# Performance work log

Measured on AMD Instinct MI355X. Metric: run time of the kernel, lower is better.

Reference implementation:

```python
import jax, jax.numpy as jnp
import numpy as np

BN, N, FIN, FO, H = 4, 2048, 128, 64, 4
D = FO * H  # 256


def setup_inputs() -> dict:
    key = jax.random.key(0)
    ks = jax.random.split(key, 13)
    rnd = lambda k, s, sc=1.0: jax.random.normal(k, s, dtype=jnp.float32) * sc
    return {
        "x": rnd(ks[0], (BN, N, FIN)),
        "adj": rnd(ks[1], (BN, N, N)),
        "W_proj": rnd(ks[2], (D, FIN), 0.08),        # xavier-ish scale
        "score_src": rnd(ks[3], (H, FO), 0.1),        # (head_num, out_features)
        "score_tgt": rnd(ks[4], (H, FO), 0.1),
        "bias_out": jnp.zeros((D,), jnp.float32),
        "w_r": rnd(ks[5], (D, D), 0.06),
        "u_r": rnd(ks[6], (D, D), 0.06),
        "w_z": rnd(ks[7], (D, D), 0.06),
        "b_wz": jnp.full((D,), -2.0, jnp.float32),    # GRUGate init_bias
        "u_z": rnd(ks[8], (D, D), 0.06),
        "w_g": rnd(ks[9], (D, D), 0.06),
        "u_g": rnd(ks[10], (D, D), 0.06),
    }


def reference(x, adj, W_proj, score_src, score_tgt, bias_out,
              w_r, u_r, w_z, b_wz, u_z, w_g, u_g):
    bn, n = x.shape[:2]
    h, fo = score_src.shape
    # eval mode: dropout is identity
    proj_flat = x @ W_proj.T                                   # (bn, n, fo*h)
    # reshape splits last dim as (fo, h): head index fastest-varying
    proj = proj_flat.reshape(bn, n, fo, h).transpose(0, 3, 1, 2)  # (bn, h, n, fo)
    residual = proj_flat                                       # (bn, n, fo*h)
    s_src = jnp.einsum('bhnf,hf->bhn', proj, score_src)
    s_tgt = jnp.einsum('bhnf,hf->bhn', proj, score_tgt)
    scores = jax.nn.leaky_relu(s_src[..., :, None] + s_tgt[..., None, :], 0.2)
    scores = scores + adj[:, None]                             # (bn, h, n, n)
    attn = jax.nn.softmax(scores, axis=-1)
    out = jnp.einsum('bhij,bhjf->bhif', attn, proj)            # (bn, h, n, fo)
    out = out.transpose(0, 2, 1, 3).reshape(bn, n, h * fo)
    # GRUGate is computed in the torch source but its result is discarded
    z = jax.nn.sigmoid(out @ w_z.T + b_wz + residual @ u_z.T)
    r = jax.nn.sigmoid(out @ w_r.T + residual @ u_r.T)
    h_hat = jnp.tanh(out @ w_g.T + (r * residual) @ u_g.T)
    _gru = (1.0 - z) * residual + z * h_hat  # unused, matches source bug
    return jax.nn.elu(out + bias_out)
```

## Files before the change

### kernel.cpp

```cpp
#include <hip/hip_runtime.h>
#include <hip/hip_bf16.h>
#include <math.h>

#define BN_   4
#define NN_   2048
#define FIN_  128
#define FO_   64
#define H_    4
#define D_    256

typedef __attribute__((ext_vector_type(8))) short bf16x8;
typedef __attribute__((ext_vector_type(4))) float floatx4;

#define LOG2E 1.4426950408889634f

#if __has_builtin(__builtin_amdgcn_exp2f)
#define EXP2(x) __builtin_amdgcn_exp2f(x)
#else
#define EXP2(x) exp2f(x)
#endif

__device__ __forceinline__ float bf2f(short u) {
    union { unsigned int i; float f; } v;
    v.i = ((unsigned int)(unsigned short)u) << 16;
    return v.f;
}
__device__ __forceinline__ short f2bf(float f) {
    union { float f; unsigned int u; } v; v.f = f;
    unsigned int r = v.u + 0x7fffu + ((v.u >> 16) & 1u);
    return (short)(unsigned short)(r >> 16);
}

#if defined(__BF16_MANT_DIG__)
typedef __bf16 bfr2 __attribute__((ext_vector_type(2)));
__device__ __forceinline__ unsigned int pack_bf16(float a, float b) {
    union { bfr2 h; unsigned int u; } v;
    v.h = (bfr2){(__bf16)a, (__bf16)b};
    return v.u;
}
#else
__device__ __forceinline__ unsigned int pack_bf16(float a, float b) {
    return ((unsigned int)(unsigned short)f2bf(a)) |
           (((unsigned int)(unsigned short)f2bf(b)) << 16);
}
#endif

__device__ __forceinline__ bf16x8 load8f(const float* __restrict__ p) {
    floatx4 a = *(const floatx4*)p;
    floatx4 b = *(const floatx4*)(p + 4);
    union { bf16x8 v; unsigned int u[4]; } r;
    r.u[0] = pack_bf16(a[0], a[1]);
    r.u[1] = pack_bf16(a[2], a[3]);
    r.u[2] = pack_bf16(b[0], b[1]);
    r.u[3] = pack_bf16(b[2], b[3]);
    return r.v;
}

__device__ __forceinline__ float score_exp(float ssv, float stv, float av) {
    float s = ssv + stv;
    s = fmaxf(s, 0.2f * s);
    return EXP2((s + av) * LOG2E);
}

__global__ __launch_bounds__(256) void proj_kernel(
    const float* __restrict__ x,
    const float* __restrict__ wproj,
    const float* __restrict__ ssrc,
    const float* __restrict__ stgt,
    short* __restrict__ pt,
    float* __restrict__ sS,
    float* __restrict__ sT,
    int b0)
{
    __shared__ short ptl[64][264];

    const int tid  = threadIdx.x;
    const int wave = tid >> 6;
    const int lane = tid & 63;
    const int l16  = lane & 15;
    const int quad = lane >> 4;

    const int b_rel = blockIdx.z;
    const int b  = b0 + b_rel;
    const int h  = blockIdx.y;
    const int j0 = blockIdx.x * 256 + wave * 64;

    floatx4 acc[4][4];
#pragma unroll
    for (int mi = 0; mi < 4; ++mi)
#pragma unroll
        for (int nj = 0; nj < 4; ++nj)
            acc[mi][nj] = (floatx4){0.f, 0.f, 0.f, 0.f};

#pragma unroll
    for (int kc = 0; kc < 4; ++kc) {
        const int c = kc * 32 + quad * 8;
        bf16x8 afr[4], bfr[4];
#pragma unroll
        for (int mi = 0; mi < 4; ++mi) {
            int f = mi * 16 + l16;
            int srow = f * H_ + h;
            afr[mi] = load8f(wproj + srow * FIN_ + c);
        }
#pragma unroll
        for (int nj = 0; nj < 4; ++nj) {
            int j = j0 + nj * 16 + l16;
            bfr[nj] = load8f(x + ((size_t)b * NN_ + j) * FIN_ + c);
        }
#pragma unroll
        for (int mi = 0; mi < 4; ++mi)
#pragma unroll
            for (int nj = 0; nj < 4; ++nj)
                acc[mi][nj] = __builtin_amdgcn_mfma_f32_16x16x32_bf16(
                    afr[mi], bfr[nj], acc[mi][nj], 0, 0, 0);
    }

#pragma unroll
    for (int mi = 0; mi < 4; ++mi)
#pragma unroll
        for (int r = 0; r < 4; ++r)
#pragma unroll
            for (int nj = 0; nj < 4; ++nj)
                ptl[mi * 16 + quad * 4 + r][wave * 64 + nj * 16 + l16] =
                    f2bf(acc[mi][nj][r]);

    float wsv[4][4], wtv[4][4];
#pragma unroll
    for (int mi = 0; mi < 4; ++mi)
#pragma unroll
        for (int r = 0; r < 4; ++r) {
            int f = mi * 16 + quad * 4 + r;
            wsv[mi][r] = ssrc[h * FO_ + f];
            wtv[mi][r] = stgt[h * FO_ + f];
        }
    const size_t sbase = ((size_t)b_rel * H_ + h) * NN_;
#pragma unroll
    for (int nj = 0; nj < 4; ++nj) {
        float ps = 0.f, pg = 0.f;
#pragma unroll
        for (int mi = 0; mi < 4; ++mi)
#pragma unroll
            for (int r = 0; r < 4; ++r) {
                ps = fmaf(wsv[mi][r], acc[mi][nj][r], ps);
                pg = fmaf(wtv[mi][r], acc[mi][nj][r], pg);
            }
        ps += __shfl_xor(ps, 16, 64); ps += __shfl_xor(ps, 32, 64);
        pg += __shfl_xor(pg, 16, 64); pg += __shfl_xor(pg, 32, 64);
        if (quad == 0) {
            int j = j0 + nj * 16 + l16;
            sS[sbase + j] = ps;
            sT[sbase + j] = pg;
        }
    }

    __syncthreads();

    const size_t base = ((size_t)b_rel * H_ + h) * (size_t)(64 * 2048)
                      + (size_t)(blockIdx.x * 8) * 2048;
#pragma unroll
    for (int p = 0; p < 8; ++p) {
        const int uid  = p * 256 + tid;
        const int mi   = (uid >> 6) & 3;
        const int l    = uid & 63;
        const int tile = uid >> 8;
        const int f    = mi * 16 + (l & 15);
        const int js   = tile * 32 + (l >> 4) * 8;
        bf16x8 v = *(const bf16x8*)&ptl[f][js];
        *(bf16x8*)&pt[base + (size_t)uid * 8] = v;
    }
}

#define RSTRIDE 65
#define WSLOT   (RSTRIDE * 16 + 16)

__global__ __launch_bounds__(512, 2) void attn_kernel(
    const float* __restrict__ adj,
    const short* __restrict__ pt,
    const float* __restrict__ sS,
    const float* __restrict__ sT,
    const float* __restrict__ bias,
    float* __restrict__ out,
    int b0)
{
    __shared__ union {
        struct {
            float adjs[8][32][36];
            float st[8][4][256];
        } m;
        float red[8][WSLOT];
    } sm;

    const int tid  = threadIdx.x;
    const int w    = tid >> 6;
    const int lane = tid & 63;
    const int l16  = lane & 15;
    const int quad = lane >> 4;
    const int r8   = lane >> 3;
    const int c4   = (lane & 7) * 4;

    int bx = blockIdx.x, bz = blockIdx.z;
    if (gridDim.z == 4 && gridDim.x == 64) {
        const int flat = bx + 64 * bz;
        const int xcd  = flat & 7;
        bz = xcd >> 1;
        bx = (xcd & 1) * 32 + (flat >> 3);
    }
    const int b_rel = bz;
    const int b  = b0 + b_rel;
    const int i0 = bx * 32;

    const short* pt2_b = pt + (size_t)b_rel * H_ * (size_t)(64 * 2048);
    const size_t sb = (size_t)b_rel * H_ * NN_;

    {
        const int t = lane * 4;
#pragma unroll
        for (int h = 0; h < 4; ++h)
            *(floatx4*)&sm.m.st[w][h][t] =
                *(const floatx4*)&sT[sb + (size_t)h * NN_ + w * 256 + t];
    }

    float ssv[2][4];
#pragma unroll
    for (int sub = 0; sub < 2; ++sub)
#pragma unroll
        for (int h = 0; h < 4; ++h)
            ssv[sub][h] = sS[sb + (size_t)h * NN_ + i0 + sub * 16 + l16];

    const float* adj_base = adj + ((size_t)b * NN_ + i0) * NN_ + w * 256;

    floatx4 acc[2][4][4];
#pragma unroll
    for (int sub = 0; sub < 2; ++sub)
#pragma unroll
        for (int h = 0; h < 4; ++h)
#pragma unroll
            for (int K = 0; K < 4; ++K)
                acc[sub][h][K] = (floatx4){0.f, 0.f, 0.f, 0.f};
    float ls[2][4] = {{0.f, 0.f, 0.f, 0.f}, {0.f, 0.f, 0.f, 0.f}};

    floatx4 ar0 = *(const floatx4*)(adj_base + (size_t)r8 * NN_ + c4);
    floatx4 ar1 = *(const floatx4*)(adj_base + (size_t)(8 + r8) * NN_ + c4);
    floatx4 ar2 = *(const floatx4*)(adj_base + (size_t)(16 + r8) * NN_ + c4);
    floatx4 ar3 = *(const floatx4*)(adj_base + (size_t)(24 + r8) * NN_ + c4);
    *(floatx4*)&sm.m.adjs[w][r8][c4]      = ar0;
    *(floatx4*)&sm.m.adjs[w][8 + r8][c4]  = ar1;
    *(floatx4*)&sm.m.adjs[w][16 + r8][c4] = ar2;
    *(floatx4*)&sm.m.adjs[w][24 + r8][c4] = ar3;

    const int lo8 = lane * 8;

#pragma unroll
    for (int jt = 0; jt < 8; ++jt) {
        const int o  = jt * 32;
        const int qo = quad * 8;

        if (jt < 7) {
            ar0 = *(const floatx4*)(adj_base + (size_t)r8 * NN_ + o + 32 + c4);
            ar1 = *(const floatx4*)(adj_base + (size_t)(8 + r8) * NN_ + o + 32 + c4);
            ar2 = *(const floatx4*)(adj_base + (size_t)(16 + r8) * NN_ + o + 32 + c4);
            ar3 = *(const floatx4*)(adj_base + (size_t)(24 + r8) * NN_ + o + 32 + c4);
        }

        floatx4 ajA[2], ajB[2];
#pragma unroll
        for (int sub = 0; sub < 2; ++sub) {
            ajA[sub] = *(const floatx4*)&sm.m.adjs[w][sub * 16 + l16][qo];
            ajB[sub] = *(const floatx4*)&sm.m.adjs[w][sub * 16 + l16][qo + 4];
        }

#pragma unroll
        for (int u = 0; u < 4; ++u) {
            const short* fb = pt2_b + ((size_t)u * 64 + (w * 8 + jt)) * 2048 + lo8;
            bf16x8 bfr[4];
#pragma unroll
            for (int K = 0; K < 4; ++K)
                bfr[K] = *(const bf16x8*)(fb + K * 512);

            const float* stp = &sm.m.st[w][u][qo];
            floatx4 stA = *(const floatx4*)(stp + o);
            floatx4 stB = *(const floatx4*)(stp + o + 4);

#pragma unroll
            for (int sub = 0; sub < 2; ++sub) {
                const float sv = ssv[sub][u];
                float w0 = score_exp(sv, stA[0], ajA[sub][0]);
                float w1 = score_exp(sv, stA[1], ajA[sub][1]);
                float w2 = score_exp(sv, stA[2], ajA[sub][2]);
                float w3 = score_exp(sv, stA[3], ajA[sub][3]);
                float w4 = score_exp(sv, stB[0], ajB[sub][0]);
                float w5 = score_exp(sv, stB[1], ajB[sub][1]);
                float w6 = score_exp(sv, stB[2], ajB[sub][2]);
                float w7 = score_exp(sv, stB[3], ajB[sub][3]);
                ls[sub][u] += ((w0 + w1) + (w2 + w3)) + ((w4 + w5) + (w6 + w7));
                union { bf16x8 v; unsigned int u4[4]; } a0;
                a0.u4[0] = pack_bf16(w0, w1);
                a0.u4[1] = pack_bf16(w2, w3);
                a0.u4[2] = pack_bf16(w4, w5);
                a0.u4[3] = pack_bf16(w6, w7);
#pragma unroll
                for (int K = 0; K < 4; ++K)
                    acc[sub][u][K] = __builtin_amdgcn_mfma_f32_16x16x32_bf16(
                        a0.v, bfr[K], acc[sub][u][K], 0, 0, 0);
            }
        }

        if (jt < 7) {
            *(floatx4*)&sm.m.adjs[w][r8][c4]      = ar0;
            *(floatx4*)&sm.m.adjs[w][8 + r8][c4]  = ar1;
            *(floatx4*)&sm.m.adjs[w][16 + r8][c4] = ar2;
            *(floatx4*)&sm.m.adjs[w][24 + r8][c4] = ar3;
        }
    }

#pragma unroll
    for (int sub = 0; sub < 2; ++sub)
#pragma unroll
        for (int h = 0; h < 4; ++h) {
            ls[sub][h] += __shfl_xor(ls[sub][h], 16, 64);
            ls[sub][h] += __shfl_xor(ls[sub][h], 32, 64);
        }

#pragma unroll
    for (int sub = 0; sub < 2; ++sub)
#pragma unroll
    for (int h = 0; h < 4; ++h) {
        __syncthreads();
#pragma unroll
        for (int K = 0; K < 4; ++K)
#pragma unroll
            for (int r = 0; r < 4; ++r)
                sm.red[w][(quad * 4 + r) * RSTRIDE + K * 16 + l16] = acc[sub][h][K][r];
        if (quad == 0)
            sm.red[w][16 * RSTRIDE + l16] = ls[sub][h];
        __syncthreads();
#pragma unroll
        for (int p = 0; p < 2; ++p) {
            int e   = tid + p * 512;
            int row = e >> 6;
            int col = e & 63;
            float s = 0.f, l = 0.f;
#pragma unroll
            for (int ww = 0; ww < 8; ++ww) {
                s += sm.red[ww][row * RSTRIDE + col];
                l += sm.red[ww][16 * RSTRIDE + row];
            }
            float v = s / l + bias[h * FO_ + col];
            v = (v > 0.f) ? v : expm1f(v);
            out[((size_t)b * NN_ + i0 + sub * 16 + row) * D_ + h * FO_ + col] = v;
        }
    }
}

extern "C" void kernel_launch(void* const* d_in, const int* in_sizes, int n_in,
                              void* d_out, int out_size, void* d_ws, size_t ws_size,
                              hipStream_t stream) {
    const float* x     = (const float*)d_in[0];
    const float* adj   = (const float*)d_in[1];
    const float* wproj = (const float*)d_in[2];
    const float* ssrc  = (const float*)d_in[3];
    const float* stgt  = (const float*)d_in[4];
    const float* bias  = (const float*)d_in[5];
    float* out = (float*)d_out;

    const size_t SLAB  = (size_t)D_ * NN_ * 2;
    const size_t SSLAB = (size_t)2 * H_ * NN_ * 4;
    int nb = (int)(ws_size / (SLAB + SSLAB));
    if (nb < 1) nb = 1;
    if (nb > 4) nb = 4;

    short* pt = (short*)d_ws;
    float* sv = (float*)((char*)d_ws + (size_t)nb * SLAB);
    float* sS = sv;
    float* sT = sv + (size_t)nb * H_ * NN_;

    for (int bb0 = 0; bb0 < BN_; bb0 += nb) {
        int cnt = (BN_ - bb0 < nb) ? (BN_ - bb0) : nb;
        proj_kernel<<<dim3(NN_ / 256, H_, cnt), 256, 0, stream>>>(
            x, wproj, ssrc, stgt, pt, sS, sT, bb0);
        attn_kernel<<<dim3(NN_ / 32, 1, cnt), 512, 0, stream>>>(
            adj, pt, sS, sT, bias, out, bb0);
    }
}
```

Before: 158.4 us.

## Retile attention blocks to 64 rows by 2 heads instead of 32 rows by 4 heads

The attention kernel now has each block cover 64 query rows and one pair of heads, with the head pair chosen by a new grid y dimension, instead of 32 rows and all four heads. Each projection fragment loaded from global memory is reused across more rows, but each adj tile is now read twice, once per head pair. The XCD remapping and the launch bound change to match the new grid, and the bound drops to one 512-thread block per CU. This trades more adj traffic and lower occupancy for less projection traffic.

```diff
diff --git a/kernel.cpp b/kernel.cpp
--- a/kernel.cpp
+++ b/kernel.cpp
@@ -173,7 +173,7 @@
 #define RSTRIDE 65
 #define WSLOT   (RSTRIDE * 16 + 16)
 
-__global__ __launch_bounds__(512, 2) void attn_kernel(
+__global__ __launch_bounds__(512, 1) void attn_kernel(
     const float* __restrict__ adj,
     const short* __restrict__ pt,
     const float* __restrict__ sS,
@@ -184,8 +184,8 @@
 {
     __shared__ union {
         struct {
-            float adjs[8][32][36];
-            float st[8][4][256];
+            float adjs[8][64][36];
+            float st[8][2][256];
         } m;
         float red[8][WSLOT];
     } sm;
@@ -198,16 +198,17 @@
     const int r8   = lane >> 3;
     const int c4   = (lane & 7) * 4;
 
-    int bx = blockIdx.x, bz = blockIdx.z;
-    if (gridDim.z == 4 && gridDim.x == 64) {
-        const int flat = bx + 64 * bz;
+    int bx = blockIdx.x, hp = blockIdx.y, bz = blockIdx.z;
+    if (gridDim.z == 4 && gridDim.x == 32 && gridDim.y == 2) {
+        const int flat = bx + 32 * hp + 64 * bz;
         const int xcd  = flat & 7;
         bz = xcd >> 1;
-        bx = (xcd & 1) * 32 + (flat >> 3);
+        hp = xcd & 1;
+        bx = flat >> 3;
     }
     const int b_rel = bz;
     const int b  = b0 + b_rel;
-    const int i0 = bx * 32;
+    const int i0 = bx * 64;
 
     const short* pt2_b = pt + (size_t)b_rel * H_ * (size_t)(64 * 2048);
     const size_t sb = (size_t)b_rel * H_ * NN_;
@@ -215,38 +216,37 @@
     {
         const int t = lane * 4;
 #pragma unroll
-        for (int h = 0; h < 4; ++h)
-            *(floatx4*)&sm.m.st[w][h][t] =
-                *(const floatx4*)&sT[sb + (size_t)h * NN_ + w * 256 + t];
-    }
-
-    float ssv[2][4];
-#pragma unroll
-    for (int sub = 0; sub < 2; ++sub)
-#pragma unroll
-        for (int h = 0; h < 4; ++h)
-            ssv[sub][h] = sS[sb + (size_t)h * NN_ + i0 + sub * 16 + l16];
+        for (int u = 0; u < 2; ++u)
+            *(floatx4*)&sm.m.st[w][u][t] =
+                *(const floatx4*)&sT[sb + (size_t)(hp * 2 + u) * NN_ + w * 256 + t];
+    }
+
+    float ssv[4][2];
+#pragma unroll
+    for (int sub = 0; sub < 4; ++sub)
+#pragma unroll
+        for (int u = 0; u < 2; ++u)
+            ssv[sub][u] = sS[sb + (size_t)(hp * 2 + u) * NN_ + i0 + sub * 16 + l16];
 
     const float* adj_base = adj + ((size_t)b * NN_ + i0) * NN_ + w * 256;
 
-    floatx4 acc[2][4][4];
-#pragma unroll
-    for (int sub = 0; sub < 2; ++sub)
-#pragma unroll
-        for (int h = 0; h < 4; ++h)
+    floatx4 acc[4][2][4];
+#pragma unroll
+    for (int sub = 0; sub < 4; ++sub)
+#pragma unroll
+        for (int u = 0; u < 2; ++u)
 #pragma unroll
             for (int K = 0; K < 4; ++K)
-                acc[sub][h][K] = (floatx4){0.f, 0.f, 0.f, 0.f};
-    float ls[2][4] = {{0.f, 0.f, 0.f, 0.f}, {0.f, 0.f, 0.f, 0.f}};
-
-    floatx4 ar0 = *(const floatx4*)(adj_base + (size_t)r8 * NN_ + c4);
-    floatx4 ar1 = *(const floatx4*)(adj_base + (size_t)(8 + r8) * NN_ + c4);
-    floatx4 ar2 = *(const floatx4*)(adj_base + (size_t)(16 + r8) * NN_ + c4);
-    floatx4 ar3 = *(const floatx4*)(adj_base + (size_t)(24 + r8) * NN_ + c4);
-    *(floatx4*)&sm.m.adjs[w][r8][c4]      = ar0;
-    *(floatx4*)&sm.m.adjs[w][8 + r8][c4]  = ar1;
-    *(floatx4*)&sm.m.adjs[w][16 + r8][c4] = ar2;
-    *(floatx4*)&sm.m.adjs[w][24 + r8][c4] = ar3;
+                acc[sub][u][K] = (floatx4){0.f, 0.f, 0.f, 0.f};
+    float ls[4][2] = {{0.f,0.f},{0.f,0.f},{0.f,0.f},{0.f,0.f}};
+
+    floatx4 ar[8];
+#pragma unroll
+    for (int g = 0; g < 8; ++g)
+        ar[g] = *(const floatx4*)(adj_base + (size_t)(g * 8 + r8) * NN_ + c4);
+#pragma unroll
+    for (int g = 0; g < 8; ++g)
+        *(floatx4*)&sm.m.adjs[w][g * 8 + r8][c4] = ar[g];
 
     const int lo8 = lane * 8;
 
@@ -256,22 +256,23 @@
         const int qo = quad * 8;
 
         if (jt < 7) {
-            ar0 = *(const floatx4*)(adj_base + (size_t)r8 * NN_ + o + 32 + c4);
-            ar1 = *(const floatx4*)(adj_base + (size_t)(8 + r8) * NN_ + o + 32 + c4);
-            ar2 = *(const floatx4*)(adj_base + (size_t)(16 + r8) * NN_ + o + 32 + c4);
-            ar3 = *(const floatx4*)(adj_base + (size_t)(24 + r8) * NN_ + o + 32 + c4);
-        }
-
-        floatx4 ajA[2], ajB[2];
-#pragma unroll
-        for (int sub = 0; sub < 2; ++sub) {
+#pragma unroll
+            for (int g = 0; g < 8; ++g)
+                ar[g] = *(const floatx4*)(adj_base + (size_t)(g * 8 + r8) * NN_
+                                          + o + 32 + c4);
+        }
+
+        floatx4 ajA[4], ajB[4];
+#pragma unroll
+        for (int sub = 0; sub < 4; ++sub) {
             ajA[sub] = *(const floatx4*)&sm.m.adjs[w][sub * 16 + l16][qo];
             ajB[sub] = *(const floatx4*)&sm.m.adjs[w][sub * 16 + l16][qo + 4];
         }
 
 #pragma unroll
-        for (int u = 0; u < 4; ++u) {
-            const short* fb = pt2_b + ((size_t)u * 64 + (w * 8 + jt)) * 2048 + lo8;
+        for (int u = 0; u < 2; ++u) {
+            const short* fb = pt2_b
+                + ((size_t)(hp * 2 + u) * 64 + (w * 8 + jt)) * 2048 + lo8;
             bf16x8 bfr[4];
 #pragma unroll
             for (int K = 0; K < 4; ++K)
@@ -282,7 +283,7 @@
             floatx4 stB = *(const floatx4*)(stp + o + 4);
 
 #pragma unroll
-            for (int sub = 0; sub < 2; ++sub) {
+            for (int sub = 0; sub < 4; ++sub) {
                 const float sv = ssv[sub][u];
                 float w0 = score_exp(sv, stA[0], ajA[sub][0]);
                 float w1 = score_exp(sv, stA[1], ajA[sub][1]);
@@ -306,34 +307,34 @@
         }
 
         if (jt < 7) {
-            *(floatx4*)&sm.m.adjs[w][r8][c4]      = ar0;
-            *(floatx4*)&sm.m.adjs[w][8 + r8][c4]  = ar1;
-            *(floatx4*)&sm.m.adjs[w][16 + r8][c4] = ar2;
-            *(floatx4*)&sm.m.adjs[w][24 + r8][c4] = ar3;
-        }
-    }
-
-#pragma unroll
-    for (int sub = 0; sub < 2; ++sub)
-#pragma unroll
-        for (int h = 0; h < 4; ++h) {
-            ls[sub][h] += __shfl_xor(ls[sub][h], 16, 64);
-            ls[sub][h] += __shfl_xor(ls[sub][h], 32, 64);
-        }
-
-#pragma unroll
-    for (int sub = 0; sub < 2; ++sub)
-#pragma unroll
-    for (int h = 0; h < 4; ++h) {
+#pragma unroll
+            for (int g = 0; g < 8; ++g)
+                *(floatx4*)&sm.m.adjs[w][g * 8 + r8][c4] = ar[g];
+        }
+    }
+
+#pragma unroll
+    for (int sub = 0; sub < 4; ++sub)
+#pragma unroll
+        for (int u = 0; u < 2; ++u) {
+            ls[sub][u] += __shfl_xor(ls[sub][u], 16, 64);
+            ls[sub][u] += __shfl_xor(ls[sub][u], 32, 64);
+        }
+
+#pragma unroll
+    for (int sub = 0; sub < 4; ++sub)
+#pragma unroll
+    for (int u = 0; u < 2; ++u) {
         __syncthreads();
 #pragma unroll
         for (int K = 0; K < 4; ++K)
 #pragma unroll
             for (int r = 0; r < 4; ++r)
-                sm.red[w][(quad * 4 + r) * RSTRIDE + K * 16 + l16] = acc[sub][h][K][r];
+                sm.red[w][(quad * 4 + r) * RSTRIDE + K * 16 + l16] = acc[sub][u][K][r];
         if (quad == 0)
-            sm.red[w][16 * RSTRIDE + l16] = ls[sub][h];
+            sm.red[w][16 * RSTRIDE + l16] = ls[sub][u];
         __syncthreads();
+        const int hh = hp * 2 + u;
 #pragma unroll
         for (int p = 0; p < 2; ++p) {
             int e   = tid + p * 512;
@@ -345,9 +346,9 @@
                 s += sm.red[ww][row * RSTRIDE + col];
                 l += sm.red[ww][16 * RSTRIDE + row];
             }
-            float v = s / l + bias[h * FO_ + col];
+            float v = s / l + bias[hh * FO_ + col];
             v = (v > 0.f) ? v : expm1f(v);
-            out[((size_t)b * NN_ + i0 + sub * 16 + row) * D_ + h * FO_ + col] = v;
+            out[((size_t)b * NN_ + i0 + sub * 16 + row) * D_ + hh * FO_ + col] = v;
         }
     }
 }
@@ -378,7 +379,7 @@
         int cnt = (BN_ - bb0 < nb) ? (BN_ - bb0) : nb;
         proj_kernel<<<dim3(NN_ / 256, H_, cnt), 256, 0, stream>>>(
             x, wproj, ssrc, stgt, pt, sS, sT, bb0);
-        attn_kernel<<<dim3(NN_ / 32, 1, cnt), 512, 0, stream>>>(
+        attn_kernel<<<dim3(NN_ / 64, 2, cnt), 512, 0, stream>>>(
             adj, pt, sS, sT, bias, out, bb0);
     }
 }
```

Result: slower. 235.7 us (+48.8%).

## Factor softmax exponentials into separable source, target and adjacency terms

Applied to the files above, without the earlier changes.

Rewrites exp(leaky_relu(s+t)+a) as max(e^s·e^t, e^{0.2s}·e^{0.2t})·e^a, which holds because exp is monotonic. The per-source and per-target exponentials are precomputed once into registers and shared memory, and the adjacency exponential is computed once per element and reused across the 4 heads. This removes most transcendental evaluations from the inner loop. In exchange it adds a second shared-memory table, which raises LDS use and the number of LDS reads. It also has no max subtraction, so very large exponents risk overflow, though the original code also had no max subtraction.

```diff
diff --git a/kernel.cpp b/kernel.cpp
--- a/kernel.cpp
+++ b/kernel.cpp
@@ -13,6 +13,7 @@
 typedef __attribute__((ext_vector_type(4))) float floatx4;
 
 #define LOG2E 1.4426950408889634f
+#define C2F   (0.2f * 1.4426950408889634f)
 
 #if __has_builtin(__builtin_amdgcn_exp2f)
 #define EXP2(x) __builtin_amdgcn_exp2f(x)
@@ -54,12 +55,6 @@
     r.u[2] = pack_bf16(b[0], b[1]);
     r.u[3] = pack_bf16(b[2], b[3]);
     return r.v;
-}
-
-__device__ __forceinline__ float score_exp(float ssv, float stv, float av) {
-    float s = ssv + stv;
-    s = fmaxf(s, 0.2f * s);
-    return EXP2((s + av) * LOG2E);
 }
 
 __global__ __launch_bounds__(256) void proj_kernel(
@@ -185,7 +180,8 @@
     __shared__ union {
         struct {
             float adjs[8][32][36];
-            float st[8][4][256];
+            float et [8][4][256];
+            float et2[8][4][256];
         } m;
         float red[8][WSLOT];
     } sm;
@@ -215,17 +211,28 @@
     {
         const int t = lane * 4;
 #pragma unroll
-        for (int h = 0; h < 4; ++h)
-            *(floatx4*)&sm.m.st[w][h][t] =
-                *(const floatx4*)&sT[sb + (size_t)h * NN_ + w * 256 + t];
-    }
-
-    float ssv[2][4];
+        for (int h = 0; h < 4; ++h) {
+            floatx4 sv = *(const floatx4*)&sT[sb + (size_t)h * NN_ + w * 256 + t];
+            floatx4 e1, e2;
+#pragma unroll
+            for (int k = 0; k < 4; ++k) {
+                e1[k] = EXP2(sv[k] * LOG2E);
+                e2[k] = EXP2(sv[k] * C2F);
+            }
+            *(floatx4*)&sm.m.et [w][h][t] = e1;
+            *(floatx4*)&sm.m.et2[w][h][t] = e2;
+        }
+    }
+
+    float es[2][4], es2[2][4];
 #pragma unroll
     for (int sub = 0; sub < 2; ++sub)
 #pragma unroll
-        for (int h = 0; h < 4; ++h)
-            ssv[sub][h] = sS[sb + (size_t)h * NN_ + i0 + sub * 16 + l16];
+        for (int h = 0; h < 4; ++h) {
+            float sv = sS[sb + (size_t)h * NN_ + i0 + sub * 16 + l16];
+            es [sub][h] = EXP2(sv * LOG2E);
+            es2[sub][h] = EXP2(sv * C2F);
+        }
 
     const float* adj_base = adj + ((size_t)b * NN_ + i0) * NN_ + w * 256;
 
@@ -262,11 +269,16 @@
             ar3 = *(const floatx4*)(adj_base + (size_t)(24 + r8) * NN_ + o + 32 + c4);
         }
 
-        floatx4 ajA[2], ajB[2];
+        floatx4 eaA[2], eaB[2];
 #pragma unroll
         for (int sub = 0; sub < 2; ++sub) {
-            ajA[sub] = *(const floatx4*)&sm.m.adjs[w][sub * 16 + l16][qo];
-            ajB[sub] = *(const floatx4*)&sm.m.adjs[w][sub * 16 + l16][qo + 4];
+            floatx4 ajA = *(const floatx4*)&sm.m.adjs[w][sub * 16 + l16][qo];
+            floatx4 ajB = *(const floatx4*)&sm.m.adjs[w][sub * 16 + l16][qo + 4];
+#pragma unroll
+            for (int k = 0; k < 4; ++k) {
+                eaA[sub][k] = EXP2(ajA[k] * LOG2E);
+                eaB[sub][k] = EXP2(ajB[k] * LOG2E);
+            }
         }
 
 #pragma unroll
@@ -277,21 +289,24 @@
             for (int K = 0; K < 4; ++K)
                 bfr[K] = *(const bf16x8*)(fb + K * 512);
 
-            const float* stp = &sm.m.st[w][u][qo];
-            floatx4 stA = *(const floatx4*)(stp + o);
-            floatx4 stB = *(const floatx4*)(stp + o + 4);
+            const float* etp  = &sm.m.et [w][u][qo];
+            const float* et2p = &sm.m.et2[w][u][qo];
+            floatx4 etA  = *(const floatx4*)(etp + o);
+            floatx4 etB  = *(const floatx4*)(etp + o + 4);
+            floatx4 et2A = *(const floatx4*)(et2p + o);
+            floatx4 et2B = *(const floatx4*)(et2p + o + 4);
 
 #pragma unroll
             for (int sub = 0; sub < 2; ++sub) {
-                const float sv = ssv[sub][u];
-                float w0 = score_exp(sv, stA[0], ajA[sub][0]);
-                float w1 = score_exp(sv, stA[1], ajA[sub][1]);
-                float w2 = score_exp(sv, stA[2], ajA[sub][2]);
-                float w3 = score_exp(sv, stA[3], ajA[sub][3]);
-                float w4 = score_exp(sv, stB[0], ajB[sub][0]);
-                float w5 = score_exp(sv, stB[1], ajB[sub][1]);
-                float w6 = score_exp(sv, stB[2], ajB[sub][2]);
-                float w7 = score_exp(sv, stB[3], ajB[sub][3]);
+                const float eu = es[sub][u], eu2 = es2[sub][u];
+                float w0 = fmaxf(eu * etA[0], eu2 * et2A[0]) * eaA[sub][0];
+                float w1 = fmaxf(eu * etA[1], eu2 * et2A[1]) * eaA[sub][1];
+                float w2 = fmaxf(eu * etA[2], eu2 * et2A[2]) * eaA[sub][2];
+                float w3 = fmaxf(eu * etA[3], eu2 * et2A[3]) * eaA[sub][3];
+                float w4 = fmaxf(eu * etB[0], eu2 * et2B[0]) * eaB[sub][0];
+                float w5 = fmaxf(eu * etB[1], eu2 * et2B[1]) * eaB[sub][1];
+                float w6 = fmaxf(eu * etB[2], eu2 * et2B[2]) * eaB[sub][2];
+                float w7 = fmaxf(eu * etB[3], eu2 * et2B[3]) * eaB[sub][3];
                 ls[sub][u] += ((w0 + w1) + (w2 + w3)) + ((w4 + w5) + (w6 + w7));
                 union { bf16x8 v; unsigned int u4[4]; } a0;
                 a0.u4[0] = pack_bf16(w0, w1);
```

After: 323.6 us. 2.04x slower.
